# Optimization experiments

Hardware: AMD Instinct MI355X
Metric: run time of the kernel (lower is better)

The kernel has to match this reference:

```python
import math
import jax, jax.numpy as jnp
import numpy as np

B, T, C, H, E, K = 2, 2048, 1024, 16, 8, 2
HID = 4 * C
D = C // H

def new_gelu(x):
    return 0.5 * x * (1.0 + jnp.tanh(math.sqrt(2.0 / math.pi) * (x + 0.044715 * x ** 3)))

def layer_norm(x, g, b, eps=1e-5):
    mu = jnp.mean(x, axis=-1, keepdims=True)
    var = jnp.var(x, axis=-1, keepdims=True)
    return (x - mu) / jnp.sqrt(var + eps) * g + b

def setup_inputs():
    key = jax.random.key(0)
    ks = jax.random.split(key, 8)
    s = 0.02
    return {
        'x': jax.random.normal(ks[0], (B, T, C), jnp.float32),
        'ln1_g': jnp.ones((C,), jnp.float32), 'ln1_b': jnp.zeros((C,), jnp.float32),
        'ln2_g': jnp.ones((C,), jnp.float32), 'ln2_b': jnp.zeros((C,), jnp.float32),
        'attn_w': (jax.random.normal(ks[1], (C, 3 * C), jnp.float32) * s),
        'attn_b': jnp.zeros((3 * C,), jnp.float32),
        'proj_w': (jax.random.normal(ks[2], (C, C), jnp.float32) * s),
        'proj_b': jnp.zeros((C,), jnp.float32),
        'router_w': (jax.random.normal(ks[3], (C, E), jnp.float32) * s),
        'fc_w': (jax.random.normal(ks[4], (E, C, HID), jnp.float32) * s),
        'fc_b': jnp.zeros((E, HID), jnp.float32),
        'pj_w': (jax.random.normal(ks[5], (E, HID, C), jnp.float32) * s),
        'pj_b': jnp.zeros((E, C), jnp.float32),
    }

def reference(x, ln1_g, ln1_b, ln2_g, ln2_b, attn_w, attn_b, proj_w, proj_b, router_w, fc_w, fc_b, pj_w, pj_b):
    # --- causal self-attention with residual ---
    h = layer_norm(x, ln1_g, ln1_b)
    qkv = h @ attn_w + attn_b                              # [B,T,3C]
    q, k, v = jnp.split(qkv, 3, axis=-1)
    q = q.reshape(B, T, H, D).transpose(0, 2, 1, 3)        # [B,H,T,D]
    k = k.reshape(B, T, H, D).transpose(0, 2, 1, 3)
    v = v.reshape(B, T, H, D).transpose(0, 2, 1, 3)
    att = jnp.einsum('bhqd,bhkd->bhqk', q, k) * (1.0 / math.sqrt(D))
    mask = jnp.tril(jnp.ones((T, T), dtype=bool))
    att = jnp.where(mask, att, jnp.float32(-jnp.inf))
    att = jax.nn.softmax(att, axis=-1)                     # dropout p=0 (eval)
    y = jnp.einsum('bhqk,bhkd->bhqd', att, v)
    y = y.transpose(0, 2, 1, 3).reshape(B, T, C)
    x = x + (y @ proj_w + proj_b)
    # --- MoE FFN with residual ---
    h2 = layer_norm(x, ln2_g, ln2_b).reshape(B * T, C)     # [N,C]
    logits = h2 @ router_w                                 # [N,E]
    probs = jax.nn.softmax(logits, axis=-1)
    topk_p, topk_i = jax.lax.top_k(probs, K)               # [N,K]
    topk_p = topk_p / jnp.sum(topk_p, axis=-1, keepdims=True)
    # dense combine weights: zero outside selected experts (same math as scatter)
    gate = jnp.zeros((B * T, E), h2.dtype).at[jnp.arange(B * T)[:, None], topk_i].add(topk_p)
    out = jnp.zeros_like(h2)
    for e in range(E):  # fixed small expert loop
        he = new_gelu(h2 @ fc_w[e] + fc_b[e])              # [N,HID]
        out = out + gate[:, e:e + 1] * (he @ pj_w[e] + pj_b[e])
    return x + out.reshape(B, T, C)
```

## Files before the change

kernel.cpp:

```cpp
#include <hip/hip_runtime.h>
#include <math.h>


typedef __bf16 b16v8 __attribute__((ext_vector_type(8)));
typedef float f32x4 __attribute__((ext_vector_type(4)));

#define MFMA(a, b, c) __builtin_amdgcn_mfma_f32_16x16x32_bf16(a, b, c, 0, 0, 0)

#define GLOAD_LDS16(g, l)                                          \
  __builtin_amdgcn_global_load_lds(                                \
      (const __attribute__((address_space(1))) void*)(g),          \
      (__attribute__((address_space(3))) void*)(l), 16, 0, 0)

constexpr int Bc = 2, Tc = 2048, Cc = 1024, Hc = 16, Dc = 64;
constexpr int Nc = Bc * Tc;
constexpr int HIDc = 4096;
constexpr int Ec = 8;
constexpr int NPAIR = Nc * 2;
constexpr int NRBMAX = NPAIR / 128 + Ec;
constexpr float LOG2E = 1.4426950408889634f;

__device__ inline unsigned short f32_bf16(float f) {
  union { float f; unsigned u; } x; x.f = f;
  unsigned r = x.u + 0x7fffu + ((x.u >> 16) & 1u);
  return (unsigned short)(r >> 16);
}

__device__ inline float gelu_f(float x) {
  float t = 2.3021188f * x * (1.f + 0.044715f * x * x);
  float e = __builtin_amdgcn_exp2f(-t);
  return x * __builtin_amdgcn_rcpf(1.f + e);
}

__device__ inline int swz(int row, int g) {
  return row * 64 + ((g ^ (row & 7)) * 8);
}

__global__ __launch_bounds__(256) void convT_kernel(
    const float* __restrict__ src, unsigned short* __restrict__ dst,
    int K, int N) {
  const size_t sb = (size_t)blockIdx.z * K * N;
  const int n0 = blockIdx.x * 32, k0 = blockIdx.y * 32;
  __shared__ float t[32][33];
  const int tx = threadIdx.x & 31, ty = threadIdx.x >> 5;
#pragma unroll
  for (int j = 0; j < 4; ++j)
    t[ty + j * 8][tx] = src[sb + (size_t)(k0 + ty + j * 8) * N + n0 + tx];
  __syncthreads();
#pragma unroll
  for (int j = 0; j < 4; ++j)
    dst[sb + (size_t)(n0 + ty + j * 8) * K + k0 + tx] = f32_bf16(t[tx][ty + j * 8]);
}

__global__ __launch_bounds__(256) void ln1_kernel(
    const float* __restrict__ x, const float* __restrict__ g,
    const float* __restrict__ b, unsigned short* __restrict__ out) {
  const int row = blockIdx.x;
  const int tid = threadIdx.x;
  const float* xr = x + (size_t)row * Cc;
  float v[4]; float s = 0.f, q = 0.f;
#pragma unroll
  for (int j = 0; j < 4; ++j) { v[j] = xr[tid + j * 256]; s += v[j]; q += v[j] * v[j]; }
#pragma unroll
  for (int m = 1; m <= 32; m <<= 1) { s += __shfl_xor(s, m); q += __shfl_xor(q, m); }
  __shared__ float red[2][4];
  const int w = tid >> 6;
  if ((tid & 63) == 0) { red[0][w] = s; red[1][w] = q; }
  __syncthreads();
  s = red[0][0] + red[0][1] + red[0][2] + red[0][3];
  q = red[1][0] + red[1][1] + red[1][2] + red[1][3];
  const float mean = s * (1.f / Cc);
  const float var = q * (1.f / Cc) - mean * mean;
  const float rstd = rsqrtf(var + 1e-5f);
#pragma unroll
  for (int j = 0; j < 4; ++j) {
    int c = tid + j * 256;
    out[(size_t)row * Cc + c] = f32_bf16((v[j] - mean) * rstd * g[c] + b[c]);
  }
}

__global__ __launch_bounds__(256) void ln2_router_kernel(
    const float* __restrict__ x, const float* __restrict__ g,
    const float* __restrict__ b, const float* __restrict__ rw,
    unsigned short* __restrict__ out, int* __restrict__ tki, float* __restrict__ tkp) {
  const int row = blockIdx.x;
  const int tid = threadIdx.x;
  const float* xr = x + (size_t)row * Cc;
  float v[4]; float s = 0.f, q = 0.f;
#pragma unroll
  for (int j = 0; j < 4; ++j) { v[j] = xr[tid + j * 256]; s += v[j]; q += v[j] * v[j]; }
#pragma unroll
  for (int m = 1; m <= 32; m <<= 1) { s += __shfl_xor(s, m); q += __shfl_xor(q, m); }
  __shared__ float red[2][4];
  const int w = tid >> 6;
  if ((tid & 63) == 0) { red[0][w] = s; red[1][w] = q; }
  __syncthreads();
  s = red[0][0] + red[0][1] + red[0][2] + red[0][3];
  q = red[1][0] + red[1][1] + red[1][2] + red[1][3];
  const float mean = s * (1.f / Cc);
  const float var = q * (1.f / Cc) - mean * mean;
  const float rstd = rsqrtf(var + 1e-5f);
  float lg[8] = {0.f, 0.f, 0.f, 0.f, 0.f, 0.f, 0.f, 0.f};
#pragma unroll
  for (int j = 0; j < 4; ++j) {
    int c = tid + j * 256;
    float nv = (v[j] - mean) * rstd * g[c] + b[c];
    out[(size_t)row * Cc + c] = f32_bf16(nv);
    const float* rwc = rw + c * 8;
#pragma unroll
    for (int e = 0; e < 8; ++e) lg[e] += nv * rwc[e];
  }
#pragma unroll
  for (int m = 1; m <= 32; m <<= 1) {
#pragma unroll
    for (int e = 0; e < 8; ++e) lg[e] += __shfl_xor(lg[e], m);
  }
  __shared__ float rl[4][8];
  if ((tid & 63) == 0) {
#pragma unroll
    for (int e = 0; e < 8; ++e) rl[w][e] = lg[e];
  }
  __syncthreads();
  if (tid == 0) {
    float L[8];
#pragma unroll
    for (int e = 0; e < 8; ++e) L[e] = rl[0][e] + rl[1][e] + rl[2][e] + rl[3][e];
    int i1 = 0;
    for (int e = 1; e < 8; ++e) if (L[e] > L[i1]) i1 = e;
    int i2 = (i1 == 0) ? 1 : 0;
    for (int e = 0; e < 8; ++e) if (e != i1 && L[e] > L[i2]) i2 = e;
    float e2 = expf(L[i2] - L[i1]);
    float inv = 1.f / (1.f + e2);
    tki[row * 2] = i1; tki[row * 2 + 1] = i2;
    tkp[row * 2] = inv; tkp[row * 2 + 1] = e2 * inv;
  }
}

__global__ __launch_bounds__(256) void count_kernel(
    const int* __restrict__ tki, int* __restrict__ counts) {
  int n = blockIdx.x * 256 + threadIdx.x;
  if (n >= Nc) return;
  atomicAdd(&counts[tki[n * 2]], 1);
  atomicAdd(&counts[tki[n * 2 + 1]], 1);
}

__global__ void scan_kernel(const int* __restrict__ counts,
                            int* __restrict__ eoff, int* __restrict__ cursor,
                            int* __restrict__ tbl_e, int* __restrict__ tbl_r0,
                            int* __restrict__ tbl_n) {
  if (threadIdx.x == 0 && blockIdx.x == 0) {
    int s = 0, nb = 0;
    for (int e = 0; e < Ec; ++e) {
      eoff[e] = s; cursor[e] = s;
      for (int r = 0; r < counts[e]; r += 128) {
        tbl_e[nb] = e; tbl_r0[nb] = r; ++nb;
      }
      s += counts[e];
    }
    eoff[Ec] = s;
    *tbl_n = nb;
  }
}

__global__ __launch_bounds__(256) void assign_kernel(
    const int* __restrict__ tki, int* __restrict__ cursor,
    int* __restrict__ slot_tok, int* __restrict__ tok2slot) {
  int n = blockIdx.x * 256 + threadIdx.x;
  if (n >= Nc) return;
#pragma unroll
  for (int kk = 0; kk < 2; ++kk) {
    int e = tki[n * 2 + kk];
    int slot = atomicAdd(&cursor[e], 1);
    slot_tok[slot] = n;
    tok2slot[n * 2 + kk] = slot;
  }
}

struct GArgs {
  const unsigned short* A;
  const unsigned short* Bt;
  const float* bias;
  int M, N, K, lda, ldb, klen;
  size_t Bstride; int biasStride;
  const int* eoff;
  const int* slot_tok;
  const int* tbl_e;
  const int* tbl_r0;
  const int* tbl_n;
  float* outF;
  const float* resid;
  unsigned short* outB;
  unsigned short* outK;
  unsigned short* outV;
};

template <int MODE>
__global__ __launch_bounds__(256) void gemm128b(GArgs g) {
  int e = 0, s0 = 0, Meff = g.M, row0;
  if constexpr (MODE == 2 || MODE == 3) {
    if ((int)blockIdx.y >= *g.tbl_n) return;
    e = g.tbl_e[blockIdx.y];
    row0 = g.tbl_r0[blockIdx.y];
    s0 = g.eoff[e];
    Meff = g.eoff[e + 1] - s0;
  } else {
    row0 = blockIdx.y * 128;
  }
  const int kh = (MODE == 3) ? blockIdx.z : 0;
  const int col0 = blockIdx.x * 128;
  const int kbase = kh * g.klen;

  __shared__ __align__(16) unsigned short As[128 * 64];
  __shared__ __align__(16) unsigned short Bs[128 * 64];

  const int tid = threadIdx.x;
  const int lane = tid & 63, w = tid >> 6;
  const int wr = w >> 1, wc = w & 1;
  const int fr = lane & 15, fg = lane >> 4;

  const unsigned short* Bt = g.Bt + (size_t)e * g.Bstride;
  const float* bias = g.bias + (size_t)e * g.biasStride;

  size_t aaddr[4], baddr[4];
#pragma unroll
  for (int i = 0; i < 4; ++i) {
    int pos = i * 256 + tid;
    int r = pos >> 3;
    int c8 = ((pos & 7) ^ (r & 7)) * 8;
    int gr = row0 + r;
    if (gr >= Meff) gr = Meff - 1;
    int srcrow;
    if constexpr (MODE == 2) srcrow = g.slot_tok[s0 + gr];
    else if constexpr (MODE == 3) srcrow = s0 + gr;
    else srcrow = gr;
    aaddr[i] = (size_t)srcrow * g.lda + kbase + c8;
    baddr[i] = (size_t)(col0 + r) * g.ldb + kbase + c8;
  }

  auto STAGE = [&](int k0) {
#pragma unroll
    for (int i = 0; i < 4; ++i) {
      GLOAD_LDS16(g.A + aaddr[i] + k0, &As[i * 2048 + w * 512]);
      GLOAD_LDS16(Bt + baddr[i] + k0, &Bs[i * 2048 + w * 512]);
    }
  };

  f32x4 acc[4][4] = {};
  const int nt = g.klen / 64;

  for (int t = 0; t < nt; ++t) {
    if (t) __syncthreads();
    STAGE(t * 64);
    __syncthreads();
    b16v8 af[4][2], bf_[4][2];
#pragma unroll
    for (int mi = 0; mi < 4; ++mi) {
      const int ar = wr * 64 + mi * 16 + fr;
      af[mi][0] = *(const b16v8*)&As[swz(ar, fg)];
      af[mi][1] = *(const b16v8*)&As[swz(ar, 4 + fg)];
    }
#pragma unroll
    for (int ni = 0; ni < 4; ++ni) {
      const int br = wc * 64 + ni * 16 + fr;
      bf_[ni][0] = *(const b16v8*)&Bs[swz(br, fg)];
      bf_[ni][1] = *(const b16v8*)&Bs[swz(br, 4 + fg)];
    }
#pragma unroll
    for (int mi = 0; mi < 4; ++mi)
#pragma unroll
      for (int ni = 0; ni < 4; ++ni) {
        acc[mi][ni] = MFMA(af[mi][0], bf_[ni][0], acc[mi][ni]);
        acc[mi][ni] = MFMA(af[mi][1], bf_[ni][1], acc[mi][ni]);
      }
  }

  float* outF3 = nullptr;
  if constexpr (MODE == 3) outF3 = g.outF + (size_t)kh * NPAIR * Cc;

#pragma unroll
  for (int mi = 0; mi < 4; ++mi) {
#pragma unroll
    for (int ni = 0; ni < 4; ++ni) {
#pragma unroll
      for (int rr = 0; rr < 4; ++rr) {
        int row = row0 + wr * 64 + mi * 16 + fg * 4 + rr;
        int col = col0 + wc * 64 + ni * 16 + fr;
        if (row >= Meff) continue;
        float bval = bias[col];
        if constexpr (MODE == 3) { if (kh != 0) bval = 0.f; }
        float val = acc[mi][ni][rr] + bval;
        if constexpr (MODE == 0) {
          int bb = row >> 11, tt = row & (Tc - 1);
          int which = col >> 10, cj = col & (Cc - 1);
          int hd = cj >> 6, d = cj & 63;
          if (which == 0)
            g.outB[(((size_t)(bb * Hc + hd)) * Tc + tt) * Dc + d] = f32_bf16(val);
          else if (which == 1)
            g.outK[(((size_t)(bb * Hc + hd)) * Tc + tt) * Dc + d] = f32_bf16(val);
          else
            g.outV[(((size_t)(bb * Hc + hd)) * Dc + d) * Tc + tt] = f32_bf16(val);
        } else if constexpr (MODE == 1) {
          size_t o = (size_t)row * g.N + col;
          g.outF[o] = val + g.resid[o];
        } else if constexpr (MODE == 2) {
          g.outB[(size_t)(s0 + row) * g.N + col] = f32_bf16(gelu_f(val));
        } else {
          outF3[(size_t)(s0 + row) * g.N + col] = val;
        }
      }
    }
  }
}

__global__ __launch_bounds__(512) void attn_kernel(
    const unsigned short* __restrict__ q, const unsigned short* __restrict__ k,
    const unsigned short* __restrict__ v, unsigned short* __restrict__ y) {
  const int qt = blockIdx.x, bh = blockIdx.y;
  const int qbase = qt * 128;
  __shared__ __align__(16) unsigned short ldsK[64][72];
  __shared__ __align__(16) unsigned short ldsVT[64][72];
  __shared__ __align__(16) unsigned short ldsP[8][16][72];
  const int tid = threadIdx.x, lane = tid & 63, w = tid >> 6;
  const int fr = lane & 15, fg = lane >> 4;
  const size_t base = (size_t)bh * Tc * Dc;
  const int qrow = qbase + w * 16 + fr;
  b16v8 qa0 = *(const b16v8*)(q + base + (size_t)qrow * Dc + fg * 8);
  b16v8 qa1 = *(const b16v8*)(q + base + (size_t)qrow * Dc + 32 + fg * 8);
  float m[4], lsum[4] = {0.f, 0.f, 0.f, 0.f};
#pragma unroll
  for (int r = 0; r < 4; ++r) m[r] = -3.0e38f;
  f32x4 oacc[4] = {};
  constexpr float SC = 0.125f * LOG2E;

  const int sr = tid >> 3, scb = (tid & 7) * 8;
  const int ntile = (qbase + 128) / 64;

  *(uint4*)&ldsK[sr][scb]  = *(const uint4*)(k + base + (size_t)sr * Dc + scb);
  *(uint4*)&ldsVT[sr][scb] = *(const uint4*)(v + base + (size_t)sr * Tc + scb);
  __syncthreads();

  for (int ti = 0; ti < ntile; ++ti) {
    const int kb = ti * 64;
    uint4 kreg, vreg;
    const bool more = (ti + 1 < ntile);
    if (more) {
      const int kn = kb + 64;
      kreg = *(const uint4*)(k + base + (size_t)(kn + sr) * Dc + scb);
      vreg = *(const uint4*)(v + base + (size_t)sr * Tc + kn + scb);
    }

    f32x4 s[4];
#pragma unroll
    for (int ni = 0; ni < 4; ++ni) {
      b16v8 kb0 = *(const b16v8*)&ldsK[ni * 16 + fr][fg * 8];
      b16v8 kb1 = *(const b16v8*)&ldsK[ni * 16 + fr][32 + fg * 8];
      f32x4 z = {};
      z = MFMA(qa0, kb0, z);
      z = MFMA(qa1, kb1, z);
      s[ni] = z;
    }
    const bool diag = (kb + 64 > qbase + w * 16);
#pragma unroll
    for (int ni = 0; ni < 4; ++ni) {
#pragma unroll
      for (int r = 0; r < 4; ++r) {
        float sv = s[ni][r] * SC;
        if (diag) {
          int gq = qbase + w * 16 + fg * 4 + r;
          int kv = kb + ni * 16 + fr;
          if (kv > gq) sv = -3.0e38f;
        }
        s[ni][r] = sv;
      }
    }
#pragma unroll
    for (int r = 0; r < 4; ++r) {
      float mx = fmaxf(fmaxf(s[0][r], s[1][r]), fmaxf(s[2][r], s[3][r]));
#pragma unroll
      for (int msk = 1; msk <= 8; msk <<= 1) mx = fmaxf(mx, __shfl_xor(mx, msk));
      float mnew = fmaxf(m[r], mx);
      float alpha = __builtin_amdgcn_exp2f(m[r] - mnew);
      float psum = 0.f;
#pragma unroll
      for (int ni = 0; ni < 4; ++ni) {
        float pp = __builtin_amdgcn_exp2f(s[ni][r] - mnew);
        s[ni][r] = pp;
        psum += pp;
      }
#pragma unroll
      for (int msk = 1; msk <= 8; msk <<= 1) psum += __shfl_xor(psum, msk);
      lsum[r] = lsum[r] * alpha + psum;
      m[r] = mnew;
#pragma unroll
      for (int ni = 0; ni < 4; ++ni) {
        oacc[ni][r] = oacc[ni][r] * alpha;
        ldsP[w][fg * 4 + r][ni * 16 + fr] = f32_bf16(s[ni][r]);
      }
    }
    asm volatile("s_waitcnt lgkmcnt(0)" ::: "memory");
    __builtin_amdgcn_sched_barrier(0);
    b16v8 pa0 = *(const b16v8*)&ldsP[w][fr][fg * 8];
    b16v8 pa1 = *(const b16v8*)&ldsP[w][fr][32 + fg * 8];
#pragma unroll
    for (int ni = 0; ni < 4; ++ni) {
      b16v8 vb0 = *(const b16v8*)&ldsVT[ni * 16 + fr][fg * 8];
      b16v8 vb1 = *(const b16v8*)&ldsVT[ni * 16 + fr][32 + fg * 8];
      oacc[ni] = MFMA(pa0, vb0, oacc[ni]);
      oacc[ni] = MFMA(pa1, vb1, oacc[ni]);
    }

    if (more) {
      __syncthreads();
      *(uint4*)&ldsK[sr][scb]  = kreg;
      *(uint4*)&ldsVT[sr][scb] = vreg;
      __syncthreads();
    }
  }

  const int bb = bh >> 4, hh = bh & 15;
#pragma unroll
  for (int r = 0; r < 4; ++r) {
    float rl = __builtin_amdgcn_rcpf(lsum[r]);
#pragma unroll
    for (int ni = 0; ni < 4; ++ni) {
      int t = qbase + w * 16 + fg * 4 + r;
      int d = ni * 16 + fr;
      y[((size_t)(bb * Tc + t)) * Cc + hh * Dc + d] = f32_bf16(oacc[ni][r] * rl);
    }
  }
}

__global__ __launch_bounds__(256) void combine_kernel(
    const float* __restrict__ pair, const float* __restrict__ tkp,
    const int* __restrict__ tok2slot, float* __restrict__ out) {
  const int n = blockIdx.x;
  const int c4 = threadIdx.x * 4;
  const int s0 = tok2slot[n * 2], s1 = tok2slot[n * 2 + 1];
  const float p0 = tkp[n * 2], p1 = tkp[n * 2 + 1];
  const float* pb = pair + (size_t)NPAIR * Cc;
  float4 a0 = *(const float4*)&pair[(size_t)s0 * Cc + c4];
  float4 a1 = *(const float4*)&pb[(size_t)s0 * Cc + c4];
  float4 b0 = *(const float4*)&pair[(size_t)s1 * Cc + c4];
  float4 b1 = *(const float4*)&pb[(size_t)s1 * Cc + c4];
  float4 o = *(float4*)&out[(size_t)n * Cc + c4];
  o.x += p0 * (a0.x + a1.x) + p1 * (b0.x + b1.x);
  o.y += p0 * (a0.y + a1.y) + p1 * (b0.y + b1.y);
  o.z += p0 * (a0.z + a1.z) + p1 * (b0.z + b1.z);
  o.w += p0 * (a0.w + a1.w) + p1 * (b0.w + b1.w);
  *(float4*)&out[(size_t)n * Cc + c4] = o;
}

extern "C" void kernel_launch(void* const* d_in, const int* in_sizes, int n_in,
                              void* d_out, int out_size, void* d_ws, size_t ws_size,
                              hipStream_t stream) {
  const float* x        = (const float*)d_in[0];
  const float* ln1_g    = (const float*)d_in[1];
  const float* ln1_b    = (const float*)d_in[2];
  const float* ln2_g    = (const float*)d_in[3];
  const float* ln2_b    = (const float*)d_in[4];
  const float* attn_w   = (const float*)d_in[5];
  const float* attn_b   = (const float*)d_in[6];
  const float* proj_w   = (const float*)d_in[7];
  const float* proj_b   = (const float*)d_in[8];
  const float* router_w = (const float*)d_in[9];
  const float* fc_w     = (const float*)d_in[10];
  const float* fc_b     = (const float*)d_in[11];
  const float* pj_w     = (const float*)d_in[12];
  const float* pj_b     = (const float*)d_in[13];
  float* out = (float*)d_out;

  char* ws = (char*)d_ws;
  size_t off = 0;
  auto alloc = [&](size_t bytes) -> void* {
    void* p = ws + off;
    off = (off + bytes + 255) & ~(size_t)255;
    return p;
  };
  unsigned short* attn_wT = (unsigned short*)alloc((size_t)3 * Cc * Cc * 2);
  unsigned short* proj_wT = (unsigned short*)alloc((size_t)Cc * Cc * 2);
  unsigned short* fc_wT   = (unsigned short*)alloc((size_t)Ec * HIDc * Cc * 2);
  unsigned short* pj_wT   = (unsigned short*)alloc((size_t)Ec * Cc * HIDc * 2);
  unsigned short* h    = (unsigned short*)alloc((size_t)Nc * Cc * 2);
  unsigned short* qb   = (unsigned short*)alloc((size_t)Nc * Cc * 2);
  unsigned short* kbuf = (unsigned short*)alloc((size_t)Nc * Cc * 2);
  unsigned short* vbuf = (unsigned short*)alloc((size_t)Nc * Cc * 2);
  unsigned short* ybuf = (unsigned short*)alloc((size_t)Nc * Cc * 2);
  unsigned short* he   = (unsigned short*)alloc((size_t)NPAIR * HIDc * 2);
  float* pairout = (float*)alloc((size_t)2 * NPAIR * Cc * 4);
  int*   tki     = (int*)alloc((size_t)Nc * 2 * 4);
  float* tkp     = (float*)alloc((size_t)Nc * 2 * 4);
  int*   counts  = (int*)alloc(Ec * 4);
  int*   eoff    = (int*)alloc((Ec + 1) * 4);
  int*   cursor  = (int*)alloc(Ec * 4);
  int*   slot_tok= (int*)alloc((size_t)NPAIR * 4);
  int*   tok2slot= (int*)alloc((size_t)Nc * 2 * 4);
  int*   tbl_e   = (int*)alloc(NRBMAX * 4);
  int*   tbl_r0  = (int*)alloc(NRBMAX * 4);
  int*   tbl_n   = (int*)alloc(4);
  (void)ws_size; (void)in_sizes; (void)n_in; (void)out_size;

  convT_kernel<<<dim3(3 * Cc / 32, Cc / 32, 1), 256, 0, stream>>>(attn_w, attn_wT, Cc, 3 * Cc);
  convT_kernel<<<dim3(Cc / 32, Cc / 32, 1), 256, 0, stream>>>(proj_w, proj_wT, Cc, Cc);
  convT_kernel<<<dim3(HIDc / 32, Cc / 32, Ec), 256, 0, stream>>>(fc_w, fc_wT, Cc, HIDc);
  convT_kernel<<<dim3(Cc / 32, HIDc / 32, Ec), 256, 0, stream>>>(pj_w, pj_wT, HIDc, Cc);

  ln1_kernel<<<Nc, 256, 0, stream>>>(x, ln1_g, ln1_b, h);

  {
    GArgs a = {};
    a.A = h; a.Bt = attn_wT; a.bias = attn_b;
    a.M = Nc; a.N = 3 * Cc; a.K = Cc; a.lda = Cc; a.ldb = Cc; a.klen = Cc;
    a.outB = qb; a.outK = kbuf; a.outV = vbuf;
    gemm128b<0><<<dim3(3 * Cc / 128, Nc / 128, 1), 256, 0, stream>>>(a);
  }

  attn_kernel<<<dim3(Tc / 128, Bc * Hc), 512, 0, stream>>>(qb, kbuf, vbuf, ybuf);

  {
    GArgs p = {};
    p.A = ybuf; p.Bt = proj_wT; p.bias = proj_b;
    p.M = Nc; p.N = Cc; p.K = Cc; p.lda = Cc; p.ldb = Cc; p.klen = Cc;
    p.outF = out; p.resid = x;
    gemm128b<1><<<dim3(Cc / 128, Nc / 128, 1), 256, 0, stream>>>(p);
  }

  ln2_router_kernel<<<Nc, 256, 0, stream>>>(out, ln2_g, ln2_b, router_w, h, tki, tkp);

  hipMemsetAsync(counts, 0, Ec * sizeof(int), stream);
  count_kernel<<<(Nc + 255) / 256, 256, 0, stream>>>(tki, counts);
  scan_kernel<<<1, 64, 0, stream>>>(counts, eoff, cursor, tbl_e, tbl_r0, tbl_n);
  assign_kernel<<<(Nc + 255) / 256, 256, 0, stream>>>(tki, cursor, slot_tok, tok2slot);

  {
    GArgs f = {};
    f.A = h; f.Bt = fc_wT; f.bias = fc_b;
    f.M = Nc; f.N = HIDc; f.K = Cc; f.lda = Cc; f.ldb = Cc; f.klen = Cc;
    f.Bstride = (size_t)HIDc * Cc; f.biasStride = HIDc;
    f.eoff = eoff; f.slot_tok = slot_tok;
    f.tbl_e = tbl_e; f.tbl_r0 = tbl_r0; f.tbl_n = tbl_n;
    f.outB = he;
    gemm128b<2><<<dim3(HIDc / 128, NRBMAX, 1), 256, 0, stream>>>(f);
  }

  {
    GArgs pj = {};
    pj.A = he; pj.Bt = pj_wT; pj.bias = pj_b;
    pj.M = Nc; pj.N = Cc; pj.K = HIDc; pj.lda = HIDc; pj.ldb = HIDc; pj.klen = HIDc / 2;
    pj.Bstride = (size_t)Cc * HIDc; pj.biasStride = Cc;
    pj.eoff = eoff;
    pj.tbl_e = tbl_e; pj.tbl_r0 = tbl_r0; pj.tbl_n = tbl_n;
    pj.outF = pairout;
    gemm128b<3><<<dim3(Cc / 128, NRBMAX, 2), 256, 0, stream>>>(pj);
  }

  combine_kernel<<<Nc, 256, 0, stream>>>(pairout, tkp, tok2slot, out);
}
```

Baseline: 636.8 us.

## Drop split-K in expert down-proj, widen weight transpose tiles, reverse attention tile order

Several unrelated changes land together. The expert down-projection GEMM no longer splits K across two halves, so the combine kernel reads one fp32 partial buffer instead of two and the workspace shrinks. The weight transpose/convert kernel moves to 64x64 tiles with float4 loads and ushort4 stores. The causal attention kernel now launches the longest query tiles first to reduce tail imbalance. Dropping split-K halves the block count of the down-proj GEMM, which may lower occupancy, in exchange for less partial-sum memory traffic.

```diff
diff --git a/kernel.cpp b/kernel.cpp
--- a/kernel.cpp
+++ b/kernel.cpp
@@ -40,16 +40,30 @@
     const float* __restrict__ src, unsigned short* __restrict__ dst,
     int K, int N) {
   const size_t sb = (size_t)blockIdx.z * K * N;
-  const int n0 = blockIdx.x * 32, k0 = blockIdx.y * 32;
-  __shared__ float t[32][33];
-  const int tx = threadIdx.x & 31, ty = threadIdx.x >> 5;
-#pragma unroll
-  for (int j = 0; j < 4; ++j)
-    t[ty + j * 8][tx] = src[sb + (size_t)(k0 + ty + j * 8) * N + n0 + tx];
+  const int n0 = blockIdx.x * 64, k0 = blockIdx.y * 64;
+  __shared__ float t[64][65];
+  const int tid = threadIdx.x;
+#pragma unroll
+  for (int j = 0; j < 4; ++j) {
+    int idx = j * 256 + tid;
+    int r = idx >> 4;
+    int c4 = (idx & 15) << 2;
+    float4 v = *(const float4*)&src[sb + (size_t)(k0 + r) * N + n0 + c4];
+    t[r][c4] = v.x; t[r][c4 + 1] = v.y; t[r][c4 + 2] = v.z; t[r][c4 + 3] = v.w;
+  }
   __syncthreads();
 #pragma unroll
-  for (int j = 0; j < 4; ++j)
-    dst[sb + (size_t)(n0 + ty + j * 8) * K + k0 + tx] = f32_bf16(t[tx][ty + j * 8]);
+  for (int j = 0; j < 4; ++j) {
+    int idx = j * 256 + tid;
+    int n = idx >> 4;
+    int k4 = (idx & 15) << 2;
+    ushort4 o;
+    o.x = f32_bf16(t[k4][n]);
+    o.y = f32_bf16(t[k4 + 1][n]);
+    o.z = f32_bf16(t[k4 + 2][n]);
+    o.w = f32_bf16(t[k4 + 3][n]);
+    *(ushort4*)&dst[sb + (size_t)(n0 + n) * K + k0 + k4] = o;
+  }
 }
 
 __global__ __launch_bounds__(256) void ln1_kernel(
@@ -206,9 +220,7 @@
   } else {
     row0 = blockIdx.y * 128;
   }
-  const int kh = (MODE == 3) ? blockIdx.z : 0;
   const int col0 = blockIdx.x * 128;
-  const int kbase = kh * g.klen;
 
   __shared__ __align__(16) unsigned short As[128 * 64];
   __shared__ __align__(16) unsigned short Bs[128 * 64];
@@ -233,8 +245,8 @@
     if constexpr (MODE == 2) srcrow = g.slot_tok[s0 + gr];
     else if constexpr (MODE == 3) srcrow = s0 + gr;
     else srcrow = gr;
-    aaddr[i] = (size_t)srcrow * g.lda + kbase + c8;
-    baddr[i] = (size_t)(col0 + r) * g.ldb + kbase + c8;
+    aaddr[i] = (size_t)srcrow * g.lda + c8;
+    baddr[i] = (size_t)(col0 + r) * g.ldb + c8;
   }
 
   auto STAGE = [&](int k0) {
@@ -274,9 +286,6 @@
       }
   }
 
-  float* outF3 = nullptr;
-  if constexpr (MODE == 3) outF3 = g.outF + (size_t)kh * NPAIR * Cc;
-
 #pragma unroll
   for (int mi = 0; mi < 4; ++mi) {
 #pragma unroll
@@ -286,9 +295,7 @@
         int row = row0 + wr * 64 + mi * 16 + fg * 4 + rr;
         int col = col0 + wc * 64 + ni * 16 + fr;
         if (row >= Meff) continue;
-        float bval = bias[col];
-        if constexpr (MODE == 3) { if (kh != 0) bval = 0.f; }
-        float val = acc[mi][ni][rr] + bval;
+        float val = acc[mi][ni][rr] + bias[col];
         if constexpr (MODE == 0) {
           int bb = row >> 11, tt = row & (Tc - 1);
           int which = col >> 10, cj = col & (Cc - 1);
@@ -305,7 +312,7 @@
         } else if constexpr (MODE == 2) {
           g.outB[(size_t)(s0 + row) * g.N + col] = f32_bf16(gelu_f(val));
         } else {
-          outF3[(size_t)(s0 + row) * g.N + col] = val;
+          g.outF[(size_t)(s0 + row) * g.N + col] = val;
         }
       }
     }
@@ -315,7 +322,8 @@
 __global__ __launch_bounds__(512) void attn_kernel(
     const unsigned short* __restrict__ q, const unsigned short* __restrict__ k,
     const unsigned short* __restrict__ v, unsigned short* __restrict__ y) {
-  const int qt = blockIdx.x, bh = blockIdx.y;
+  const int qt = gridDim.x - 1 - blockIdx.x;
+  const int bh = blockIdx.y;
   const int qbase = qt * 128;
   __shared__ __align__(16) unsigned short ldsK[64][72];
   __shared__ __align__(16) unsigned short ldsVT[64][72];
@@ -437,16 +445,13 @@
   const int c4 = threadIdx.x * 4;
   const int s0 = tok2slot[n * 2], s1 = tok2slot[n * 2 + 1];
   const float p0 = tkp[n * 2], p1 = tkp[n * 2 + 1];
-  const float* pb = pair + (size_t)NPAIR * Cc;
-  float4 a0 = *(const float4*)&pair[(size_t)s0 * Cc + c4];
-  float4 a1 = *(const float4*)&pb[(size_t)s0 * Cc + c4];
-  float4 b0 = *(const float4*)&pair[(size_t)s1 * Cc + c4];
-  float4 b1 = *(const float4*)&pb[(size_t)s1 * Cc + c4];
+  float4 a = *(const float4*)&pair[(size_t)s0 * Cc + c4];
+  float4 b = *(const float4*)&pair[(size_t)s1 * Cc + c4];
   float4 o = *(float4*)&out[(size_t)n * Cc + c4];
-  o.x += p0 * (a0.x + a1.x) + p1 * (b0.x + b1.x);
-  o.y += p0 * (a0.y + a1.y) + p1 * (b0.y + b1.y);
-  o.z += p0 * (a0.z + a1.z) + p1 * (b0.z + b1.z);
-  o.w += p0 * (a0.w + a1.w) + p1 * (b0.w + b1.w);
+  o.x += p0 * a.x + p1 * b.x;
+  o.y += p0 * a.y + p1 * b.y;
+  o.z += p0 * a.z + p1 * b.z;
+  o.w += p0 * a.w + p1 * b.w;
   *(float4*)&out[(size_t)n * Cc + c4] = o;
 }
 
@@ -486,7 +491,7 @@
   unsigned short* vbuf = (unsigned short*)alloc((size_t)Nc * Cc * 2);
   unsigned short* ybuf = (unsigned short*)alloc((size_t)Nc * Cc * 2);
   unsigned short* he   = (unsigned short*)alloc((size_t)NPAIR * HIDc * 2);
-  float* pairout = (float*)alloc((size_t)2 * NPAIR * Cc * 4);
+  float* pairout = (float*)alloc((size_t)NPAIR * Cc * 4);
   int*   tki     = (int*)alloc((size_t)Nc * 2 * 4);
   float* tkp     = (float*)alloc((size_t)Nc * 2 * 4);
   int*   counts  = (int*)alloc(Ec * 4);
@@ -499,10 +504,10 @@
   int*   tbl_n   = (int*)alloc(4);
   (void)ws_size; (void)in_sizes; (void)n_in; (void)out_size;
 
-  convT_kernel<<<dim3(3 * Cc / 32, Cc / 32, 1), 256, 0, stream>>>(attn_w, attn_wT, Cc, 3 * Cc);
-  convT_kernel<<<dim3(Cc / 32, Cc / 32, 1), 256, 0, stream>>>(proj_w, proj_wT, Cc, Cc);
-  convT_kernel<<<dim3(HIDc / 32, Cc / 32, Ec), 256, 0, stream>>>(fc_w, fc_wT, Cc, HIDc);
-  convT_kernel<<<dim3(Cc / 32, HIDc / 32, Ec), 256, 0, stream>>>(pj_w, pj_wT, HIDc, Cc);
+  convT_kernel<<<dim3(3 * Cc / 64, Cc / 64, 1), 256, 0, stream>>>(attn_w, attn_wT, Cc, 3 * Cc);
+  convT_kernel<<<dim3(Cc / 64, Cc / 64, 1), 256, 0, stream>>>(proj_w, proj_wT, Cc, Cc);
+  convT_kernel<<<dim3(HIDc / 64, Cc / 64, Ec), 256, 0, stream>>>(fc_w, fc_wT, Cc, HIDc);
+  convT_kernel<<<dim3(Cc / 64, HIDc / 64, Ec), 256, 0, stream>>>(pj_w, pj_wT, HIDc, Cc);
 
   ln1_kernel<<<Nc, 256, 0, stream>>>(x, ln1_g, ln1_b, h);
 
@@ -545,12 +550,12 @@
   {
     GArgs pj = {};
     pj.A = he; pj.Bt = pj_wT; pj.bias = pj_b;
-    pj.M = Nc; pj.N = Cc; pj.K = HIDc; pj.lda = HIDc; pj.ldb = HIDc; pj.klen = HIDc / 2;
+    pj.M = Nc; pj.N = Cc; pj.K = HIDc; pj.lda = HIDc; pj.ldb = HIDc; pj.klen = HIDc;
     pj.Bstride = (size_t)Cc * HIDc; pj.biasStride = Cc;
-    pj.eoff = eoff;
+    pj.eoff = eoff; pj.slot_tok = slot_tok;
     pj.tbl_e = tbl_e; pj.tbl_r0 = tbl_r0; pj.tbl_n = tbl_n;
     pj.outF = pairout;
-    gemm128b<3><<<dim3(Cc / 128, NRBMAX, 2), 256, 0, stream>>>(pj);
+    gemm128b<3><<<dim3(Cc / 128, NRBMAX, 1), 256, 0, stream>>>(pj);
   }
 
   combine_kernel<<<Nc, 256, 0, stream>>>(pairout, tkp, tok2slot, out);
```

Result: faster. 616.5 us (-3.2%).
